# Kernel optimization log

Hardware: AMD Instinct MI355X
Metric: run time of the kernel (lower is better)

Reference implementation:

```python
import jax, jax.numpy as jnp
import numpy as np

EPS = 1e-12  # matches torch F.normalize eps

def _l2norm(x):
    n = jnp.linalg.norm(x, axis=-1, keepdims=True)
    return x / jnp.maximum(n, EPS)

def setup_inputs() -> dict:
    key = jax.random.key(0)
    k1, k2, k3, k4, k5 = jax.random.split(key, 5)
    B, S, D, V, N = 8, 512, 128, 100000, 2048
    query_embeddings = jax.random.normal(k1, (B, S, D), dtype=jnp.float32)
    key_embeddings = jax.random.normal(k2, (V, D), dtype=jnp.float32)
    batch_idx = jax.random.randint(k3, (N, 1), 0, B)
    seq_idx = jax.random.randint(k4, (N, 1), 0, S)
    label_locations = jnp.concatenate([batch_idx, seq_idx], axis=1).astype(jnp.int64)
    labels = jax.random.randint(k5, (N,), 0, V).astype(jnp.int64)
    return {"query_embeddings": query_embeddings, "key_embeddings": key_embeddings,
            "label_locations": label_locations, "labels": labels}

def reference(query_embeddings, key_embeddings, label_locations, labels):
    # gather supervised positions: [N, D]
    q = query_embeddings[label_locations[:, 0], label_locations[:, 1]]
    q = _l2norm(q)
    k = _l2norm(key_embeddings)
    logits = jnp.einsum('nd,vd->nv', q, k)  # [N, V]
    # mean-reduced softmax cross entropy
    logz = jax.nn.logsumexp(logits, axis=-1)  # [N]
    tgt = jnp.take_along_axis(logits, labels[:, None], axis=-1)[:, 0]
    return jnp.mean(logz - tgt)
```

## Files before the change

### kernel.cpp

```cpp
#include <hip/hip_runtime.h>
#include <hip/hip_bf16.h>

typedef __attribute__((ext_vector_type(8))) short short8;
typedef __attribute__((ext_vector_type(4))) float f32x4;

namespace {
constexpr int D    = 128;
constexpr int SEQ  = 512;
constexpr int NV   = 100000;
constexpr int NN   = 2048;
constexpr int KC   = 64;
constexpr int CHUNK_B = KC * D * 2;
constexpr int NCHUNK  = (NV + KC - 1) / KC;
constexpr int CPS     = 13;
constexpr int NSLICE  = (NCHUNK + CPS - 1) / CPS;
constexpr int MBLKS   = 8;
constexpr float LOG2E = 1.4426950408889634f;
constexpr float EPSN  = 1e-12f;
}

__global__ void prep_kernel(const float* __restrict__ qemb,
                            const float* __restrict__ kemb,
                            const int*   __restrict__ loc,
                            __hip_bfloat16* __restrict__ Kn,
                            __hip_bfloat16* __restrict__ Qn)
{
    int wave = (blockIdx.x * blockDim.x + threadIdx.x) >> 6;
    int lane = threadIdx.x & 63;
    if (wave >= NV + NN) return;

    const float* src;
    __hip_bfloat16* dst;
    float extra;
    if (wave < NV) {
        src = kemb + (size_t)wave * D;
        dst = Kn + (size_t)wave * D;
        extra = 1.0f;
    } else {
        int n = wave - NV;
        int b = loc[2 * n], s = loc[2 * n + 1];
        src = qemb + ((size_t)b * SEQ + s) * D;
        dst = Qn + (size_t)n * D;
        extra = LOG2E;
    }
    float2 v = *(const float2*)(src + lane * 2);
    float ss = v.x * v.x + v.y * v.y;
    #pragma unroll
    for (int m = 1; m < 64; m <<= 1) ss += __shfl_xor(ss, m);
    float inv = extra / fmaxf(sqrtf(ss), EPSN);
    __hip_bfloat162 o;
    o.x = __float2bfloat16(v.x * inv);
    o.y = __float2bfloat16(v.y * inv);
    *(__hip_bfloat162*)(dst + lane * 2) = o;
}

__global__ __launch_bounds__(512, 4)
void lse_main(const __hip_bfloat16* __restrict__ Kn,
              const __hip_bfloat16* __restrict__ Qn,
              float* __restrict__ sums)
{
    __shared__ char lds[2 * CHUNK_B];
    const int tid  = threadIdx.x;
    const int lane = tid & 63;
    const int lr   = lane & 15;
    const int lh   = lane >> 4;
    const int w    = tid >> 6;

    const int bid = blockIdx.x;
    const int lin = (bid & 7) * NSLICE + (bid >> 3);
    const int slice = lin >> 3;
    const int mblk  = lin & 7;

    const int chunk0 = slice * CPS;
    const int nch = min(CPS, NCHUNK - chunk0);
    const int m0 = mblk * 256 + w * 32;
    const char* kbase = (const char*)Kn;

    auto stage = [&](int c, int bi) {
        const int keybase = (chunk0 + c) * KC;
        #pragma unroll
        for (int r = 0; r < 2; ++r) {
            const int i   = w * 2 + r;
            const int kic = i * 4 + lh;
            const int key = min(keybase + kic, NV - 1);
            const int sb  = (lr ^ (kic & 7)) << 4;
            const char* g = kbase + (size_t)key * 256 + sb;
            const char* l = lds + bi * CHUNK_B + i * 1024;
            __builtin_amdgcn_global_load_lds(
                (const __attribute__((address_space(1))) void*)g,
                (__attribute__((address_space(3))) void*)l, 16, 0, 0);
        }
    };

    stage(0, 0);

    short8 qf[2][4];
    #pragma unroll
    for (int rg = 0; rg < 2; ++rg)
        #pragma unroll
        for (int ds = 0; ds < 4; ++ds)
            qf[rg][ds] = *(const short8*)((const short*)Qn +
                          (size_t)(m0 + rg * 16 + lr) * D + ds * 32 + lh * 8);

    float rowsum[2][4] = {};
    __syncthreads();

    int cur = 0;
    for (int c = 0; c < nch; ++c) {
        if (c + 1 < nch) stage(c + 1, cur ^ 1);

        const char* buf = lds + cur * CHUNK_B;
        const int vbase = (chunk0 + c) * KC;
        const bool full = (vbase + KC <= NV);
        #pragma unroll
        for (int kg = 0; kg < 4; ++kg) {
            const int kic = kg * 16 + lr;
            const int rx  = (kic & 7) << 4;
            f32x4 acc[2] = {{0,0,0,0},{0,0,0,0}};
            #pragma unroll
            for (int ds2 = 0; ds2 < 4; ++ds2) {
                short8 bf = *(const short8*)(buf +
                              ((kic * 256 + ds2 * 64 + lh * 16) ^ rx));
                #pragma unroll
                for (int rg = 0; rg < 2; ++rg)
                    acc[rg] = __builtin_amdgcn_mfma_f32_16x16x32_bf16(
                                  qf[rg][ds2], bf, acc[rg], 0, 0, 0);
            }
            if (full) {
                #pragma unroll
                for (int rg = 0; rg < 2; ++rg)
                    #pragma unroll
                    for (int j = 0; j < 4; ++j)
                        rowsum[rg][j] += __builtin_amdgcn_exp2f(acc[rg][j]);
            } else {
                const bool ok = (vbase + kic) < NV;
                #pragma unroll
                for (int rg = 0; rg < 2; ++rg)
                    #pragma unroll
                    for (int j = 0; j < 4; ++j)
                        rowsum[rg][j] += ok ? __builtin_amdgcn_exp2f(acc[rg][j]) : 0.f;
            }
        }
        __syncthreads();
        cur ^= 1;
    }

    #pragma unroll
    for (int rg = 0; rg < 2; ++rg)
        #pragma unroll
        for (int j = 0; j < 4; ++j) {
            float v = rowsum[rg][j];
            v += __shfl_xor(v, 1);
            v += __shfl_xor(v, 2);
            v += __shfl_xor(v, 4);
            v += __shfl_xor(v, 8);
            if (lr == 0)
                atomicAdd(&sums[m0 + rg * 16 + lh * 4 + j], v);
        }
}

__global__ void tgt_kernel(const float* __restrict__ qemb,
                           const float* __restrict__ kemb,
                           const int*   __restrict__ loc,
                           const int*   __restrict__ labels,
                           float* __restrict__ tgt)
{
    int n = (blockIdx.x * blockDim.x + threadIdx.x) >> 6;
    int lane = threadIdx.x & 63;
    if (n >= NN) return;
    int b = loc[2 * n], s = loc[2 * n + 1];
    const float* q = qemb + ((size_t)b * SEQ + s) * D;
    const float* k = kemb + (size_t)labels[n] * D;
    float2 qv = *(const float2*)(q + lane * 2);
    float2 kv = *(const float2*)(k + lane * 2);
    float qq = qv.x * qv.x + qv.y * qv.y;
    float kk = kv.x * kv.x + kv.y * kv.y;
    float qk = qv.x * kv.x + qv.y * kv.y;
    #pragma unroll
    for (int m = 1; m < 64; m <<= 1) {
        qq += __shfl_xor(qq, m);
        kk += __shfl_xor(kk, m);
        qk += __shfl_xor(qk, m);
    }
    if (lane == 0)
        tgt[n] = qk / (fmaxf(sqrtf(qq), EPSN) * fmaxf(sqrtf(kk), EPSN));
}

__global__ void final_kernel(const float* __restrict__ sums,
                             const float* __restrict__ tgt,
                             float* __restrict__ out)
{
    __shared__ float wsum[4];
    int t = threadIdx.x;
    float acc = 0.f;
    for (int n = t; n < NN; n += 256)
        acc += logf(sums[n]) - tgt[n];
    #pragma unroll
    for (int m = 1; m < 64; m <<= 1) acc += __shfl_xor(acc, m);
    if ((t & 63) == 0) wsum[t >> 6] = acc;
    __syncthreads();
    if (t == 0) out[0] = (wsum[0] + wsum[1] + wsum[2] + wsum[3]) / (float)NN;
}

extern "C" void kernel_launch(void* const* d_in, const int* in_sizes, int n_in,
                              void* d_out, int out_size, void* d_ws, size_t ws_size,
                              hipStream_t stream)
{
    const float* qemb   = (const float*)d_in[0];
    const float* kemb   = (const float*)d_in[1];
    const int*   loc    = (const int*)d_in[2];
    const int*   labels = (const int*)d_in[3];
    float* out = (float*)d_out;

    char* ws = (char*)d_ws;
    __hip_bfloat16* Kn = (__hip_bfloat16*)ws;
    size_t off = (size_t)NV * D * 2;
    __hip_bfloat16* Qn = (__hip_bfloat16*)(ws + off);
    off += (size_t)NN * D * 2;
    float* sums = (float*)(ws + off); off += (size_t)NN * 4;
    float* tgt  = (float*)(ws + off); off += (size_t)NN * 4;

    hipMemsetAsync(sums, 0, NN * sizeof(float), stream);

    {
        int waves  = NV + NN;
        int blocks = (waves + 3) / 4;
        prep_kernel<<<blocks, 256, 0, stream>>>(qemb, kemb, loc, Kn, Qn);
    }
    lse_main<<<MBLKS * NSLICE, 512, 0, stream>>>(Kn, Qn, sums);
    tgt_kernel<<<(NN * 64 + 255) / 256, 256, 0, stream>>>(qemb, kemb, loc, labels, tgt);
    final_kernel<<<1, 256, 0, stream>>>(sums, tgt, out);
}
```

Measured before the change: 167.8 us.

## Triple-buffer key chunks with partial vmcnt wait and widen prep loads

The main LSE kernel moves from double to triple buffering of key chunks in LDS. It prefetches two chunks ahead and replaces the full __syncthreads with an s_waitcnt vmcnt(2) plus a barrier, so the next chunk's loads can stay in flight across iterations. Chunks per slice grow from 13 to 17, which means fewer blocks and atomics, though LDS use per block rises to three chunks and may lower occupancy. The prep kernel now has each half-wave normalize one row with float4 loads and 8-byte stores, halving the launched waves.

```diff
diff --git a/kernel.cpp b/kernel.cpp
--- a/kernel.cpp
+++ b/kernel.cpp
@@ -2,6 +2,7 @@
 #include <hip/hip_bf16.h>
 
 typedef __attribute__((ext_vector_type(8))) short short8;
+typedef __attribute__((ext_vector_type(4))) short short4v;
 typedef __attribute__((ext_vector_type(4))) float f32x4;
 
 namespace {
@@ -12,46 +13,53 @@
 constexpr int KC   = 64;
 constexpr int CHUNK_B = KC * D * 2;
 constexpr int NCHUNK  = (NV + KC - 1) / KC;
-constexpr int CPS     = 13;
+constexpr int CPS     = 17;
 constexpr int NSLICE  = (NCHUNK + CPS - 1) / CPS;
 constexpr int MBLKS   = 8;
 constexpr float LOG2E = 1.4426950408889634f;
 constexpr float EPSN  = 1e-12f;
 }
 
-__global__ void prep_kernel(const float* __restrict__ qemb,
-                            const float* __restrict__ kemb,
-                            const int*   __restrict__ loc,
-                            __hip_bfloat16* __restrict__ Kn,
-                            __hip_bfloat16* __restrict__ Qn)
-{
-    int wave = (blockIdx.x * blockDim.x + threadIdx.x) >> 6;
-    int lane = threadIdx.x & 63;
-    if (wave >= NV + NN) return;
+__global__ __launch_bounds__(256)
+void prep_kernel(const float* __restrict__ qemb,
+                 const float* __restrict__ kemb,
+                 const int*   __restrict__ loc,
+                 __hip_bfloat16* __restrict__ Kn,
+                 __hip_bfloat16* __restrict__ Qn)
+{
+    const int gw   = (blockIdx.x * blockDim.x + threadIdx.x) >> 6;
+    const int lane = threadIdx.x & 63;
+    const int half = lane >> 5;
+    const int l32  = lane & 31;
+    const int row  = gw * 2 + half;
+    if (row >= NV + NN) return;
 
     const float* src;
     __hip_bfloat16* dst;
     float extra;
-    if (wave < NV) {
-        src = kemb + (size_t)wave * D;
-        dst = Kn + (size_t)wave * D;
+    if (row < NV) {
+        src = kemb + (size_t)row * D;
+        dst = Kn + (size_t)row * D;
         extra = 1.0f;
     } else {
-        int n = wave - NV;
+        int n = row - NV;
         int b = loc[2 * n], s = loc[2 * n + 1];
         src = qemb + ((size_t)b * SEQ + s) * D;
         dst = Qn + (size_t)n * D;
         extra = LOG2E;
     }
-    float2 v = *(const float2*)(src + lane * 2);
-    float ss = v.x * v.x + v.y * v.y;
-    #pragma unroll
-    for (int m = 1; m < 64; m <<= 1) ss += __shfl_xor(ss, m);
+    float4 v = *(const float4*)(src + l32 * 4);
+    float ss = v.x * v.x + v.y * v.y + v.z * v.z + v.w * v.w;
+    #pragma unroll
+    for (int m = 1; m < 32; m <<= 1) ss += __shfl_xor(ss, m);
     float inv = extra / fmaxf(sqrtf(ss), EPSN);
-    __hip_bfloat162 o;
-    o.x = __float2bfloat16(v.x * inv);
-    o.y = __float2bfloat16(v.y * inv);
-    *(__hip_bfloat162*)(dst + lane * 2) = o;
+
+    union { __hip_bfloat162 h2[2]; short4v s4; } u;
+    u.h2[0].x = __float2bfloat16(v.x * inv);
+    u.h2[0].y = __float2bfloat16(v.y * inv);
+    u.h2[1].x = __float2bfloat16(v.z * inv);
+    u.h2[1].y = __float2bfloat16(v.w * inv);
+    *(short4v*)((char*)dst + l32 * 8) = u.s4;
 }
 
 __global__ __launch_bounds__(512, 4)
@@ -59,7 +67,7 @@
               const __hip_bfloat16* __restrict__ Qn,
               float* __restrict__ sums)
 {
-    __shared__ char lds[2 * CHUNK_B];
+    __shared__ char lds[3 * CHUNK_B];
     const int tid  = threadIdx.x;
     const int lane = tid & 63;
     const int lr   = lane & 15;
@@ -93,6 +101,7 @@
     };
 
     stage(0, 0);
+    if (nch > 1) stage(1, 1);
 
     short8 qf[2][4];
     #pragma unroll
@@ -105,11 +114,10 @@
     float rowsum[2][4] = {};
     __syncthreads();
 
-    int cur = 0;
     for (int c = 0; c < nch; ++c) {
-        if (c + 1 < nch) stage(c + 1, cur ^ 1);
-
-        const char* buf = lds + cur * CHUNK_B;
+        if (c + 2 < nch) stage(c + 2, (c + 2) % 3);
+
+        const char* buf = lds + (c % 3) * CHUNK_B;
         const int vbase = (chunk0 + c) * KC;
         const bool full = (vbase + KC <= NV);
         #pragma unroll
@@ -141,8 +149,9 @@
                         rowsum[rg][j] += ok ? __builtin_amdgcn_exp2f(acc[rg][j]) : 0.f;
             }
         }
-        __syncthreads();
-        cur ^= 1;
+        asm volatile("s_waitcnt vmcnt(2)" ::: "memory");
+        __builtin_amdgcn_s_barrier();
+        asm volatile("" ::: "memory");
     }
 
     #pragma unroll
@@ -223,7 +232,7 @@
     hipMemsetAsync(sums, 0, NN * sizeof(float), stream);
 
     {
-        int waves  = NV + NN;
+        int waves  = (NV + NN + 1) / 2;
         int blocks = (waves + 3) / 4;
         prep_kernel<<<blocks, 256, 0, stream>>>(qemb, kemb, loc, Kn, Qn);
     }
```

Measured after the change: 161.0 us. 4.0% less time.
